# Optimization experiments

Hardware: AMD Instinct MI355X
Metric: run time of the kernel (lower is better)

The kernel has to match this reference:

```python
import jax, jax.numpy as jnp
import numpy as np

EPS = 1e-5

def instance_norm(x):
    # x: [B, n, C]; InstanceNorm1d normalizes over the n (length) axis per channel, no affine
    mean = jnp.mean(x, axis=1, keepdims=True)
    var = jnp.var(x, axis=1, keepdims=True)  # biased variance, matches torch
    return (x - mean) / jnp.sqrt(var + EPS)

def gat_layer(h, w, a_src, a_dst, b):
    # h: [B, n, d_in]; w: [H, d_in, d_out]; a_src/a_dst: [H, d_out, 1]; b: [d_out]
    h_ = jnp.einsum('bnd,hdk->bhnk', h, w)               # [B, H, n, d_out]
    s_src = jnp.einsum('bhnk,hk->bhn', h_, a_src[..., 0])  # [B, H, n]
    s_dst = jnp.einsum('bhnk,hk->bhn', h_, a_dst[..., 0])  # [B, H, n]
    attn = s_src[:, :, :, None] + s_dst[:, :, None, :]    # [B, H, n, n]
    attn = jax.nn.leaky_relu(attn, negative_slope=0.2)
    attn = jax.nn.softmax(attn, axis=-1)
    return jnp.einsum('bhnm,bhmk->bhnk', attn, h_) + b    # [B, H, n, d_out]

def setup_inputs() -> dict:
    key = jax.random.key(0)
    ks = jax.random.split(key, 7)
    B, N = 4, 4096
    x = jax.random.normal(ks[0], (B, N, 64), dtype=jnp.float32)
    g = 1.414
    def xavier(k, shape):
        fan_in, fan_out = shape[-2], shape[-1]
        lim = g * np.sqrt(6.0 / (fan_in + fan_out))
        return jax.random.uniform(k, shape, jnp.float32, -lim, lim)
    return {
        'x': x,
        'w0': xavier(ks[1], (4, 64, 32)),
        'a_src0': xavier(ks[2], (4, 32, 1)),
        'a_dst0': xavier(ks[3], (4, 32, 1)),
        'b0': jnp.zeros((32,), jnp.float32),
        'w1': xavier(ks[4], (1, 128, 64)),
        'a_src1': xavier(ks[5], (1, 64, 1)),
        'a_dst1': xavier(ks[6], (1, 64, 1)),
        'b1': jnp.zeros((64,), jnp.float32),
    }

def reference(x, w0, a_src0, a_dst0, b0, w1, a_src1, a_dst1, b1):
    B, N = x.shape[:2]
    # layer 0: norm -> GAT(4 heads) -> concat heads -> ELU
    h = instance_norm(x)
    h = gat_layer(h, w0, a_src0, a_dst0, b0)              # [B, 4, N, 32]
    h = jnp.transpose(h, (0, 2, 1, 3)).reshape(B, N, -1)  # [B, N, 128]
    h = jax.nn.elu(h)
    # layer 1: norm -> GAT(1 head) -> squeeze head
    h = instance_norm(h)
    h = gat_layer(h, w1, a_src1, a_dst1, b1)              # [B, 1, N, 64]
    return h[:, 0]                                        # [B, N, 64]
```

## Files before the change

### kernel.cpp

```cpp
#include <hip/hip_runtime.h>
#include <math.h>

#define N_ 4096

static constexpr size_t OFF_HP0    = 2048;
static constexpr size_t OFF_ELU    = 2048;
static constexpr size_t OFF_SS0    = 2099200;
static constexpr size_t OFF_SD0    = 2164736;
static constexpr size_t OFF_RUNS0  = 2230272;
static constexpr size_t OFF_SV0    = 2361344;
static constexpr size_t OFF_PM0    = 2426880;
static constexpr size_t OFF_EP0    = 2492416;
static constexpr size_t OFF_EN0    = 2557952;
static constexpr size_t OFF_CPP0   = 2623488;
static constexpr size_t OFF_CPN0   = 2689040;
static constexpr size_t OFF_TPP0   = 3279904;
static constexpr size_t OFF_TPN0   = 5377568;
static constexpr size_t OFF_HP1    = 3279904;
static constexpr size_t OFF_SS1    = 4328480;
static constexpr size_t OFF_SD1    = 4344864;
static constexpr size_t OFF_RUNS1  = 4361248;
static constexpr size_t OFF_SV1    = 4394016;
static constexpr size_t OFF_PM1    = 4410400;
static constexpr size_t OFF_EP1    = 4426784;
static constexpr size_t OFF_EN1    = 4443168;
static constexpr size_t OFF_CPP1   = 4459552;
static constexpr size_t OFF_CPN1   = 4475940;
static constexpr size_t OFF_TPP1   = 4754984;
static constexpr size_t OFF_TPN1   = 5803816;
static constexpr size_t OFF_S0P    = 7475232;
static constexpr size_t OFF_S1P    = 7491616;
static constexpr size_t OFF_RAWP0  = 7524384;
static constexpr size_t OFF_RAWN0  = 7786528;
static constexpr size_t OFF_BP0    = 8048672;
static constexpr size_t OFF_BN0    = 8311328;
static constexpr size_t OFF_RAWP1  = 8573984;
static constexpr size_t OFF_RAWN1  = 8705056;
static constexpr size_t OFF_BP1    = 8836128;
static constexpr size_t OFF_BN1    = 8967456;

__device__ __forceinline__ unsigned f2s(float f){
  unsigned u=__float_as_uint(f);
  return u^((u&0x80000000u)?0xFFFFFFFFu:0x80000000u);
}
__device__ __forceinline__ float s2f(unsigned s){
  unsigned u=(s&0x80000000u)?(s^0x80000000u):~s;
  return __uint_as_float(u);
}
__device__ __forceinline__ void fma4(float4& a, float s, float4 w){
  a.x+=s*w.x; a.y+=s*w.y; a.z+=s*w.z; a.w+=s*w.w;
}
__device__ __forceinline__ float dot4(float4 a, float4 b){
  return a.x*b.x+a.y*b.y+a.z*b.z+a.w*b.w;
}

template<int C>
__global__ void kstats(const float* __restrict__ x, float* __restrict__ statsP){
  int blk=blockIdx.x; int b=blk>>5;
  int tid=threadIdx.x;
  const int RPT=256/C;
  const int IT=128/RPT;
  int c=tid%C, rl=tid/C;
  const float* xb=x+(size_t)b*N_*C;
  float s1=0.f,s2=0.f;
  int r0=(blk&31)*128+rl;
  for(int i=0;i<IT;i++){
    float v=xb[(size_t)(r0+i*RPT)*C+c];
    s1+=v;s2+=v*v;
  }
  __shared__ float sh1[256],sh2[256];
  sh1[tid]=s1;sh2[tid]=s2;__syncthreads();
  if(tid<C){
    float a1=0.f,a2=0.f;
    for(int g=0;g<RPT;g++){a1+=sh1[g*C+tid];a2+=sh2[g*C+tid];}
    statsP[((size_t)blk*C+tid)*2+0]=a1;
    statsP[((size_t)blk*C+tid)*2+1]=a2;
  }
}

__global__ void __launch_bounds__(256) kproj0(
                       const float* __restrict__ x, const float* __restrict__ statsP,
                       const float* __restrict__ w0, const float* __restrict__ asrc,
                       const float* __restrict__ adst, float* __restrict__ hp,
                       float* __restrict__ ss, float* __restrict__ sd){
  __shared__ float4 w4[512];
  __shared__ float mean[64],rstd[64];
  __shared__ float red1[256],red2[256];
  __shared__ float ssP[1024],sdP[1024];
  int tid=threadIdx.x;
  int blk=blockIdx.x;
  int b=blk>>6, h=(blk>>4)&3, nb=blk&15;
  const float4* wg=(const float4*)w0+(size_t)h*512;
  w4[tid]=wg[tid]; w4[tid+256]=wg[tid+256];
  {
    int tc=tid&63, tg=tid>>6;
    float a1=0.f,a2=0.f;
    #pragma unroll 2
    for(int g=tg*8;g<tg*8+8;g++){
      a1+=statsP[((size_t)(b*32+g)*64+tc)*2+0];
      a2+=statsP[((size_t)(b*32+g)*64+tc)*2+1];
    }
    red1[tid]=a1; red2[tid]=a2;
  }
  __syncthreads();
  if(tid<64){
    float s1=red1[tid]+red1[tid+64]+red1[tid+128]+red1[tid+192];
    float s2=red2[tid]+red2[tid+64]+red2[tid+128]+red2[tid+192];
    float mu=s1*(1.0f/N_);
    float var=s2*(1.0f/N_)-mu*mu;
    mean[tid]=mu; rstd[tid]=rsqrtf(var+1e-5f);
  }
  __syncthreads();
  int w=tid>>6, lane=tid&63;
  int n0=nb*256+lane;
  const float4* xb=(const float4*)(x+((size_t)b*N_+n0)*64);
  float4 acc[4][2];
  #pragma unroll
  for(int r=0;r<4;r++){acc[r][0]=make_float4(0,0,0,0);acc[r][1]=make_float4(0,0,0,0);}
  for(int ch=0;ch<8;ch++){
    float4 wr[8][2];
    #pragma unroll
    for(int dd=0;dd<8;dd++){
      wr[dd][0]=w4[(ch*8+dd)*8+w*2+0];
      wr[dd][1]=w4[(ch*8+dd)*8+w*2+1];
    }
    float4 mn0=*(const float4*)&mean[ch*8], mn1=*(const float4*)&mean[ch*8+4];
    float4 rs0=*(const float4*)&rstd[ch*8], rs1=*(const float4*)&rstd[ch*8+4];
    #pragma unroll
    for(int r=0;r<4;r++){
      float4 t0=xb[(size_t)r*1024+ch*2+0];
      float4 t1=xb[(size_t)r*1024+ch*2+1];
      float hv[8];
      hv[0]=(t0.x-mn0.x)*rs0.x; hv[1]=(t0.y-mn0.y)*rs0.y;
      hv[2]=(t0.z-mn0.z)*rs0.z; hv[3]=(t0.w-mn0.w)*rs0.w;
      hv[4]=(t1.x-mn1.x)*rs1.x; hv[5]=(t1.y-mn1.y)*rs1.y;
      hv[6]=(t1.z-mn1.z)*rs1.z; hv[7]=(t1.w-mn1.w)*rs1.w;
      #pragma unroll
      for(int dd=0;dd<8;dd++){
        fma4(acc[r][0],hv[dd],wr[dd][0]);
        fma4(acc[r][1],hv[dd],wr[dd][1]);
      }
    }
  }
  float4 a1v0=((const float4*)asrc)[h*8+w*2+0];
  float4 a1v1=((const float4*)asrc)[h*8+w*2+1];
  float4 a2v0=((const float4*)adst)[h*8+w*2+0];
  float4 a2v1=((const float4*)adst)[h*8+w*2+1];
  int p=b*4+h;
  #pragma unroll
  for(int r=0;r<4;r++){
    ssP[w*256+r*64+lane]=dot4(acc[r][0],a1v0)+dot4(acc[r][1],a1v1);
    sdP[w*256+r*64+lane]=dot4(acc[r][0],a2v0)+dot4(acc[r][1],a2v1);
    float4* o4=(float4*)(hp+((size_t)p*N_+n0+r*64)*32+w*8);
    o4[0]=acc[r][0]; o4[1]=acc[r][1];
  }
  __syncthreads();
  {
    float s=ssP[tid]+ssP[256+tid]+ssP[512+tid]+ssP[768+tid];
    float d=sdP[tid]+sdP[256+tid]+sdP[512+tid]+sdP[768+tid];
    ss[(size_t)p*N_+nb*256+tid]=s;
    sd[(size_t)p*N_+nb*256+tid]=d;
  }
}

__global__ void __launch_bounds__(256) kproj1(
                       const float* __restrict__ x, const float* __restrict__ statsP,
                       const float* __restrict__ w1, const float* __restrict__ asrc,
                       const float* __restrict__ adst, float* __restrict__ hp,
                       float* __restrict__ ss, float* __restrict__ sd){
  __shared__ float4 w4[512];
  __shared__ float wa[128],wd[128],mean[128],rstd[128];
  __shared__ float red1[256],red2[256];
  int tid=threadIdx.x;
  int blk=blockIdx.x;
  int b=blk>>6, cgq=(blk>>4)&3, nb=blk&15;
  {
    const float4* wg=(const float4*)w1;
    int i=tid;       int d=i>>2, c=i&3; w4[i]=wg[d*16+cgq*4+c];
    i=tid+256;       d=i>>2;     c=i&3; w4[i]=wg[d*16+cgq*4+c];
  }
  {
    int tc=tid&127, tg=tid>>7;
    float a1=0.f,a2=0.f;
    #pragma unroll 4
    for(int g=tg*16;g<tg*16+16;g++){
      a1+=statsP[((size_t)(b*32+g)*128+tc)*2+0];
      a2+=statsP[((size_t)(b*32+g)*128+tc)*2+1];
    }
    red1[tid]=a1; red2[tid]=a2;
  }
  __syncthreads();
  if(tid<128){
    float s1a=0.f,s2a=0.f;
    for(int k=0;k<64;k++){float wv=w1[tid*64+k];s1a+=wv*asrc[k];s2a+=wv*adst[k];}
    wa[tid]=s1a;wd[tid]=s2a;
    float s1=red1[tid]+red1[tid+128];
    float s2=red2[tid]+red2[tid+128];
    float mu=s1*(1.0f/N_);
    float var=s2*(1.0f/N_)-mu*mu;
    mean[tid]=mu; rstd[tid]=rsqrtf(var+1e-5f);
  }
  __syncthreads();
  int w=tid>>6, lane=tid&63;
  int cg=cgq*4+w;
  int n0=nb*256+lane;
  const float4* xb=(const float4*)(x+((size_t)b*N_+n0)*128);
  float4 acc[4];
  #pragma unroll
  for(int r=0;r<4;r++) acc[r]=make_float4(0,0,0,0);
  float s1a[4]={0.f,0.f,0.f,0.f}, s2a[4]={0.f,0.f,0.f,0.f};
  bool dosum=(cgq==0)&&(w==0);
  for(int ch=0;ch<16;ch++){
    float4 wr[8];
    #pragma unroll
    for(int dd=0;dd<8;dd++) wr[dd]=w4[(ch*8+dd)*4+w];
    float4 mn0=*(const float4*)&mean[ch*8], mn1=*(const float4*)&mean[ch*8+4];
    float4 rs0=*(const float4*)&rstd[ch*8], rs1=*(const float4*)&rstd[ch*8+4];
    float4 wa0,wa1,wd0,wd1;
    if(dosum){
      wa0=*(const float4*)&wa[ch*8]; wa1=*(const float4*)&wa[ch*8+4];
      wd0=*(const float4*)&wd[ch*8]; wd1=*(const float4*)&wd[ch*8+4];
    }
    #pragma unroll
    for(int r=0;r<4;r++){
      float4 t0=xb[(size_t)r*2048+ch*2+0];
      float4 t1=xb[(size_t)r*2048+ch*2+1];
      float hv[8];
      hv[0]=(t0.x-mn0.x)*rs0.x; hv[1]=(t0.y-mn0.y)*rs0.y;
      hv[2]=(t0.z-mn0.z)*rs0.z; hv[3]=(t0.w-mn0.w)*rs0.w;
      hv[4]=(t1.x-mn1.x)*rs1.x; hv[5]=(t1.y-mn1.y)*rs1.y;
      hv[6]=(t1.z-mn1.z)*rs1.z; hv[7]=(t1.w-mn1.w)*rs1.w;
      #pragma unroll
      for(int dd=0;dd<8;dd++) fma4(acc[r],hv[dd],wr[dd]);
      if(dosum){
        s1a[r]+=hv[0]*wa0.x+hv[1]*wa0.y+hv[2]*wa0.z+hv[3]*wa0.w
               +hv[4]*wa1.x+hv[5]*wa1.y+hv[6]*wa1.z+hv[7]*wa1.w;
        s2a[r]+=hv[0]*wd0.x+hv[1]*wd0.y+hv[2]*wd0.z+hv[3]*wd0.w
               +hv[4]*wd1.x+hv[5]*wd1.y+hv[6]*wd1.z+hv[7]*wd1.w;
      }
    }
  }
  #pragma unroll
  for(int r=0;r<4;r++){
    float4* o4=(float4*)(hp+((size_t)b*N_+n0+r*64)*64+cg*4);
    o4[0]=acc[r];
  }
  if(dosum){
    #pragma unroll
    for(int r=0;r<4;r++){
      ss[(size_t)b*N_+n0+r*64]=s1a[r];
      sd[(size_t)b*N_+n0+r*64]=s2a[r];
    }
  }
}

__global__ void __launch_bounds__(512) ksort_runs(const float* __restrict__ sdst,
                                                  unsigned long long* __restrict__ runs){
  __shared__ unsigned long long sm[1024];
  int p=blockIdx.x>>2, run=blockIdx.x&3;
  int tid=threadIdx.x;
  const float* s=sdst+(size_t)p*N_+run*1024;
  for(int l=tid;l<1024;l+=512){
    unsigned key=f2s(s[l]);
    sm[l]=((unsigned long long)key<<32)|(unsigned)(run*1024+l);
  }
  for(unsigned k=2;k<=1024u;k<<=1)
    for(unsigned j=k>>1;j>0;j>>=1){
      __syncthreads();
      unsigned t=(unsigned)tid;
      unsigned i=((t&~(j-1))<<1)|(t&(j-1));
      unsigned q=i|j;
      bool up=((i&k)==0);
      unsigned long long a=sm[i],b=sm[q];
      if((a>b)==up){sm[i]=b;sm[q]=a;}
    }
  __syncthreads();
  unsigned long long* rg=runs+(size_t)p*N_+run*1024;
  for(int l=tid;l<1024;l+=512) rg[l]=sm[l];
}

__global__ void __launch_bounds__(1024) kmerge(const unsigned long long* __restrict__ runs,
    float* __restrict__ sv, unsigned* __restrict__ perm,
    float* __restrict__ eP, float* __restrict__ eN){
  __shared__ unsigned long long sm[4096];
  int p=blockIdx.x>>2, cg=blockIdx.x&3;
  int tid=threadIdx.x;
  const unsigned long long* rg=runs+(size_t)p*N_;
  for(int l=tid;l<4096;l+=1024) sm[l]=rg[l];
  __syncthreads();
  unsigned long long e=sm[cg*1024+tid];
  int rank=tid;
  #pragma unroll
  for(int o=0;o<4;o++){
    if(o==cg) continue;
    const unsigned long long* base=sm+o*1024;
    int lo=0,hi=1024;
    while(lo<hi){int mid=(lo+hi)>>1; if(base[mid]<e) lo=mid+1; else hi=mid;}
    rank+=lo;
  }
  unsigned long long mk=sm[1023];
  if(sm[2047]>mk) mk=sm[2047];
  if(sm[3071]>mk) mk=sm[3071];
  if(sm[4095]>mk) mk=sm[4095];
  float m=s2f((unsigned)(mk>>32));
  float v=s2f((unsigned)(e>>32));
  size_t o=(size_t)p*N_+rank;
  sv[o]=v;
  perm[o]=(unsigned)(e&0xffffffffu);
  eP[o]=expf(v-m);
  eN[o]=expf(0.2f*(v-m));
}

__device__ __forceinline__ void counts_block(const float* __restrict__ eP,
    const float* __restrict__ eN, float* __restrict__ CPP, float* __restrict__ CPN,
    int p, float* s){
  int t=threadIdx.x;
  for(int pass=0;pass<2;pass++){
    const float* e=pass?eN:eP;
    float* C=pass?CPN:CPP;
    const float4* e4=(const float4*)(e+(size_t)p*N_);
    float4 a0=e4[t*4+0],a1=e4[t*4+1],a2=e4[t*4+2],a3=e4[t*4+3];
    float lp=a0.x+a0.y+a0.z+a0.w+a1.x+a1.y+a1.z+a1.w
            +a2.x+a2.y+a2.z+a2.w+a3.x+a3.y+a3.z+a3.w;
    if(pass) __syncthreads();
    s[t]=lp; __syncthreads();
    for(int off=1;off<256;off<<=1){
      float tv=(t>=off)?s[t-off]:0.f;
      __syncthreads();
      s[t]+=tv;
      __syncthreads();
    }
    float bp=s[t]-lp;
    size_t o=(size_t)p*4097+(size_t)t*16;
    C[o+ 0]=bp; bp+=a0.x; C[o+ 1]=bp; bp+=a0.y; C[o+ 2]=bp; bp+=a0.z; C[o+ 3]=bp; bp+=a0.w;
    C[o+ 4]=bp; bp+=a1.x; C[o+ 5]=bp; bp+=a1.y; C[o+ 6]=bp; bp+=a1.z; C[o+ 7]=bp; bp+=a1.w;
    C[o+ 8]=bp; bp+=a2.x; C[o+ 9]=bp; bp+=a2.y; C[o+10]=bp; bp+=a2.z; C[o+11]=bp; bp+=a2.w;
    C[o+12]=bp; bp+=a3.x; C[o+13]=bp; bp+=a3.y; C[o+14]=bp; bp+=a3.z; C[o+15]=bp;
    if(t==255) C[(size_t)p*4097+4096]=s[255];
  }
}

__global__ void __launch_bounds__(256) ktables0(const unsigned* __restrict__ perm,
    const float* __restrict__ eP, const float* __restrict__ eN,
    const float* __restrict__ hp, float* __restrict__ TPP, float* __restrict__ TPN,
    float* __restrict__ rawP, float* __restrict__ rawN,
    float* __restrict__ CPP, float* __restrict__ CPN){
  __shared__ float s[256];
  if(blockIdx.x<16){ counts_block(eP,eN,CPP,CPN,blockIdx.x,s); return; }
  int gw=((blockIdx.x-16)*256+threadIdx.x)>>6;
  int lane=threadIdx.x&63, half=lane>>5, ch=lane&31;
  int cglob=gw*2+half;
  int p=cglob>>9, c=cglob&511;
  float aP=0.f,aN=0.f;
  #pragma unroll
  for(int q=0;q<8;q++){
    int r=c*8+q;
    size_t ro=(size_t)p*N_+r;
    float ep=eP[ro],en=eN[ro];
    unsigned pr=perm[ro];
    float hv=hp[((size_t)p*N_+pr)*32+ch];
    size_t to=((size_t)p*4097+r)*32+ch;
    TPP[to]=aP; TPN[to]=aN;
    aP+=ep*hv; aN+=en*hv;
  }
  size_t bo=((size_t)p*512+c)*32+ch;
  rawP[bo]=aP; rawN[bo]=aN;
}

__global__ void __launch_bounds__(256) ktables1(const unsigned* __restrict__ perm,
    const float* __restrict__ eP, const float* __restrict__ eN,
    const float* __restrict__ hp, float* __restrict__ TPP, float* __restrict__ TPN,
    float* __restrict__ rawP, float* __restrict__ rawN,
    float* __restrict__ CPP, float* __restrict__ CPN){
  __shared__ float s[256];
  if(blockIdx.x<4){ counts_block(eP,eN,CPP,CPN,blockIdx.x,s); return; }
  int wid=((blockIdx.x-4)*256+threadIdx.x)>>6;
  int lane=threadIdx.x&63;
  int p=wid>>9, c=wid&511;
  float aP=0.f,aN=0.f;
  #pragma unroll
  for(int q=0;q<8;q++){
    int r=c*8+q;
    size_t ro=(size_t)p*N_+r;
    float ep=eP[ro],en=eN[ro];
    unsigned pr=perm[ro];
    float hv=hp[((size_t)p*N_+pr)*64+lane];
    size_t to=((size_t)p*4097+r)*64+lane;
    TPP[to]=aP; TPN[to]=aN;
    aP+=ep*hv; aN+=en*hv;
  }
  size_t bo=((size_t)p*512+c)*64+lane;
  rawP[bo]=aP; rawN[bo]=aN;
}

template<int D>
__global__ void __launch_bounds__(256) kscan(const float* __restrict__ rawP,
    const float* __restrict__ rawN, float* __restrict__ bP, float* __restrict__ bN,
    float* __restrict__ TPP, float* __restrict__ TPN){
  __shared__ float ssum[256];
  int p=blockIdx.x>>1, pass=blockIdx.x&1;
  const float* src=pass?rawN:rawP;
  float* dst=pass?bN:bP;
  float* tp=pass?TPN:TPP;
  int tid=threadIdx.x;
  constexpr int SEG=256/D;
  constexpr int CPS=512/SEG;
  int ch=tid&(D-1), sg=tid/D;
  const float* s0=src+(size_t)p*512*D;
  float acc=0.f;
  for(int c=sg*CPS;c<sg*CPS+CPS;c++) acc+=s0[(size_t)c*D+ch];
  ssum[tid]=acc; __syncthreads();
  float base=0.f, tot=0.f;
  #pragma unroll
  for(int g=0;g<SEG;g++){float v=ssum[g*D+ch]; tot+=v; if(g<sg) base+=v;}
  float r=base;
  for(int c=sg*CPS;c<sg*CPS+CPS;c++){
    dst[((size_t)p*513+c)*D+ch]=r;
    r+=s0[(size_t)c*D+ch];
  }
  if(sg==0){
    dst[((size_t)p*513+512)*D+ch]=0.f;
    tp[((size_t)p*4097+4096)*D+ch]=tot;
  }
}

__global__ void __launch_bounds__(256) keval0(const float* __restrict__ ss,
                       const float* __restrict__ sv,
                       const float* __restrict__ bP, const float* __restrict__ bN,
                       const float* __restrict__ TPP, const float* __restrict__ TPN,
                       const float* __restrict__ CPP, const float* __restrict__ CPN,
                       const float* __restrict__ bias, float* __restrict__ out){
  __shared__ float svl[4128];
  __shared__ float ssl[32];
  int tid=threadIdx.x, blk=blockIdx.x;
  int p=blk>>7, i0=(blk&127)*32;
  int b=p>>2, h=p&3;
  const float* svp=sv+(size_t)p*N_;
  for(int j=tid;j<4096;j+=256) svl[j+(j>>7)]=svp[j];
  if(tid<32) ssl[tid]=ss[(size_t)p*N_+i0+tid];
  __syncthreads();
  int lane=tid&63, half=lane>>5, ch=lane&31;
  float bch=bias[ch];
  float m=svl[4126];
  float tot=TPP[((size_t)p*4097+4096)*32+ch];
  float CT =CPP[(size_t)p*4097+4096];
  for(int pass=0;pass<4;pass++){
    int rloc=pass*8+(tid>>5);
    int i=i0+rloc;
    float ssrc=ssl[rloc];
    float xx=ssrc+m;
    float M=xx>0.f?xx:0.2f*xx;
    float fpos=expf(xx-M),fneg=expf(0.2f*xx-M);
    float th=-ssrc;
    float s1v=svl[ch*129+127];
    unsigned long long bal=__ballot(s1v<=th);
    int c1=half?(int)__popcll(bal>>32):(int)__popcll(bal&0xFFFFFFFFull);
    int lo;
    if(c1>=32){ lo=4096; }
    else{
      float s2v=svl[c1*129+ch*4+3];
      unsigned long long bal2=__ballot(s2v<=th);
      int c2=half?(int)__popcll(bal2>>32):(int)__popcll(bal2&0xFFFFFFFFull);
      int base=c1*128+c2*4;
      int bi=base+c1;
      float q0=svl[bi],q1=svl[bi+1],q2=svl[bi+2],q3=svl[bi+3];
      int c3=(q0<=th)+(q1<=th)+(q2<=th)+(q3<=th);
      lo=base+c3;
    }
    int c=lo>>3;
    float relP=TPP[((size_t)p*4097+lo)*32+ch];
    float relN=TPN[((size_t)p*4097+lo)*32+ch];
    float baP=bP[((size_t)p*513+c)*32+ch];
    float baN=bN[((size_t)p*513+c)*32+ch];
    float CPl=CPP[(size_t)p*4097+lo];
    float CNl=CPN[(size_t)p*4097+lo];
    float denom=fpos*(CT-CPl)+fneg*CNl;
    float v=fpos*(tot-(baP+relP))+fneg*(baN+relN);
    float r=v/denom+bch;
    r=r>0.f?r:expm1f(r);
    out[((size_t)(b*N_+i))*128+h*32+ch]=r;
  }
}

__global__ void __launch_bounds__(256) keval1(const float* __restrict__ ss,
                       const float* __restrict__ sv,
                       const float* __restrict__ bP, const float* __restrict__ bN,
                       const float* __restrict__ TPP, const float* __restrict__ TPN,
                       const float* __restrict__ CPP, const float* __restrict__ CPN,
                       const float* __restrict__ bias, float* __restrict__ out){
  __shared__ float svl[4160];
  __shared__ float ssl[32];
  int tid=threadIdx.x, blk=blockIdx.x;
  int p=blk>>7, i0=(blk&127)*32;
  const float* svp=sv+(size_t)p*N_;
  for(int j=tid;j<4096;j+=256) svl[j+(j>>6)]=svp[j];
  if(tid<32) ssl[tid]=ss[(size_t)p*N_+i0+tid];
  __syncthreads();
  int lane=tid&63;
  float bch=bias[lane];
  float m=svl[4158];
  float tot=TPP[((size_t)p*4097+4096)*64+lane];
  float CT =CPP[(size_t)p*4097+4096];
  for(int pass=0;pass<8;pass++){
    int rloc=pass*4+(tid>>6);
    int i=i0+rloc;
    float ssrc=ssl[rloc];
    float xx=ssrc+m;
    float M=xx>0.f?xx:0.2f*xx;
    float fpos=expf(xx-M),fneg=expf(0.2f*xx-M);
    float th=-ssrc;
    float s1v=svl[lane*65+63];
    int c1=(int)__popcll(__ballot(s1v<=th));
    int lo;
    if(c1>=64){ lo=4096; }
    else{
      float s2v=svl[c1*65+lane];
      lo=c1*64+(int)__popcll(__ballot(s2v<=th));
    }
    int c=lo>>3;
    float relP=TPP[((size_t)p*4097+lo)*64+lane];
    float relN=TPN[((size_t)p*4097+lo)*64+lane];
    float baP=bP[((size_t)p*513+c)*64+lane];
    float baN=bN[((size_t)p*513+c)*64+lane];
    float CPl=CPP[(size_t)p*4097+lo];
    float CNl=CPN[(size_t)p*4097+lo];
    float denom=fpos*(CT-CPl)+fneg*CNl;
    float v=fpos*(tot-(baP+relP))+fneg*(baN+relN);
    out[((size_t)p*N_+i)*64+lane]=v/denom+bch;
  }
}

extern "C" void kernel_launch(void* const* d_in, const int* in_sizes, int n_in,
                              void* d_out, int out_size, void* d_ws, size_t ws_size,
                              hipStream_t stream) {
  const float* x  =(const float*)d_in[0];
  const float* w0 =(const float*)d_in[1];
  const float* as0=(const float*)d_in[2];
  const float* ad0=(const float*)d_in[3];
  const float* b0 =(const float*)d_in[4];
  const float* w1 =(const float*)d_in[5];
  const float* as1=(const float*)d_in[6];
  const float* ad1=(const float*)d_in[7];
  const float* b1 =(const float*)d_in[8];
  float* ws=(float*)d_ws;
  float* out=(float*)d_out;

  float* s0p = ws+OFF_S0P;
  float* s1p = ws+OFF_S1P;
  float* hp0 = ws+OFF_HP0;
  float* elu = ws+OFF_ELU;
  float* ss0 = ws+OFF_SS0;  float* sd0 = ws+OFF_SD0;
  unsigned long long* runs0=(unsigned long long*)(ws+OFF_RUNS0);
  float* sv0 = ws+OFF_SV0;
  unsigned* pm0=(unsigned*)(ws+OFF_PM0);
  float* eP0 = ws+OFF_EP0;  float* eN0 = ws+OFF_EN0;
  float* cP0 = ws+OFF_CPP0; float* cN0 = ws+OFF_CPN0;
  float* rP0 = ws+OFF_RAWP0; float* rN0 = ws+OFF_RAWN0;
  float* bP0 = ws+OFF_BP0;  float* bN0 = ws+OFF_BN0;
  float* tP0 = ws+OFF_TPP0; float* tN0 = ws+OFF_TPN0;
  float* hp1 = ws+OFF_HP1;
  float* ss1 = ws+OFF_SS1;  float* sd1 = ws+OFF_SD1;
  unsigned long long* runs1=(unsigned long long*)(ws+OFF_RUNS1);
  float* sv1 = ws+OFF_SV1;
  unsigned* pm1=(unsigned*)(ws+OFF_PM1);
  float* eP1 = ws+OFF_EP1;  float* eN1 = ws+OFF_EN1;
  float* cP1 = ws+OFF_CPP1; float* cN1 = ws+OFF_CPN1;
  float* rP1 = ws+OFF_RAWP1; float* rN1 = ws+OFF_RAWN1;
  float* bP1 = ws+OFF_BP1;  float* bN1 = ws+OFF_BN1;
  float* tP1 = ws+OFF_TPP1; float* tN1 = ws+OFF_TPN1;

  kstats<64><<<128,256,0,stream>>>(x,s0p);
  kproj0<<<256,256,0,stream>>>(x,s0p,w0,as0,ad0,hp0,ss0,sd0);
  ksort_runs<<<64,512,0,stream>>>(sd0,runs0);
  kmerge<<<64,1024,0,stream>>>(runs0,sv0,pm0,eP0,eN0);
  ktables0<<<1040,256,0,stream>>>(pm0,eP0,eN0,hp0,tP0,tN0,rP0,rN0,cP0,cN0);
  kscan<32><<<32,256,0,stream>>>(rP0,rN0,bP0,bN0,tP0,tN0);
  keval0<<<2048,256,0,stream>>>(ss0,sv0,bP0,bN0,tP0,tN0,cP0,cN0,b0,elu);
  kstats<128><<<128,256,0,stream>>>(elu,s1p);
  kproj1<<<256,256,0,stream>>>(elu,s1p,w1,as1,ad1,hp1,ss1,sd1);
  ksort_runs<<<16,512,0,stream>>>(sd1,runs1);
  kmerge<<<16,1024,0,stream>>>(runs1,sv1,pm1,eP1,eN1);
  ktables1<<<516,256,0,stream>>>(pm1,eP1,eN1,hp1,tP1,tN1,rP1,rN1,cP1,cN1);
  kscan<64><<<8,256,0,stream>>>(rP1,rN1,bP1,bN1,tP1,tN1);
  keval1<<<512,256,0,stream>>>(ss1,sv1,bP1,bN1,tP1,tN1,cP1,cN1,b1,out);
}
```

Before: 192.7 us.

## Interleave P/N prefix tables as float2 and fuse layer-1 stats into keval0

After: 207.0 us. +7.4%, slower.

```diff
diff --git a/kernel.cpp b/kernel.cpp
--- a/kernel.cpp
+++ b/kernel.cpp
@@ -12,10 +12,8 @@
 static constexpr size_t OFF_PM0    = 2426880;
 static constexpr size_t OFF_EP0    = 2492416;
 static constexpr size_t OFF_EN0    = 2557952;
-static constexpr size_t OFF_CPP0   = 2623488;
-static constexpr size_t OFF_CPN0   = 2689040;
-static constexpr size_t OFF_TPP0   = 3279904;
-static constexpr size_t OFF_TPN0   = 5377568;
+static constexpr size_t OFF_CP0    = 2623488;
+static constexpr size_t OFF_TP0    = 3279904;
 static constexpr size_t OFF_HP1    = 3279904;
 static constexpr size_t OFF_SS1    = 4328480;
 static constexpr size_t OFF_SD1    = 4344864;
@@ -24,20 +22,14 @@
 static constexpr size_t OFF_PM1    = 4410400;
 static constexpr size_t OFF_EP1    = 4426784;
 static constexpr size_t OFF_EN1    = 4443168;
-static constexpr size_t OFF_CPP1   = 4459552;
-static constexpr size_t OFF_CPN1   = 4475940;
-static constexpr size_t OFF_TPP1   = 4754984;
-static constexpr size_t OFF_TPN1   = 5803816;
+static constexpr size_t OFF_CP1    = 4459552;
+static constexpr size_t OFF_TP1    = 4754984;
 static constexpr size_t OFF_S0P    = 7475232;
-static constexpr size_t OFF_S1P    = 7491616;
-static constexpr size_t OFF_RAWP0  = 7524384;
-static constexpr size_t OFF_RAWN0  = 7786528;
-static constexpr size_t OFF_BP0    = 8048672;
-static constexpr size_t OFF_BN0    = 8311328;
-static constexpr size_t OFF_RAWP1  = 8573984;
-static constexpr size_t OFF_RAWN1  = 8705056;
-static constexpr size_t OFF_BP1    = 8836128;
-static constexpr size_t OFF_BN1    = 8967456;
+static constexpr size_t OFF_RAW0   = 7524384;
+static constexpr size_t OFF_B0     = 8048672;
+static constexpr size_t OFF_RAW1   = 8573984;
+static constexpr size_t OFF_B1     = 8836128;
+static constexpr size_t OFF_EVP    = 9098784;
 
 __device__ __forceinline__ unsigned f2s(float f){
   unsigned u=__float_as_uint(f);
@@ -164,7 +156,7 @@
 }
 
 __global__ void __launch_bounds__(256) kproj1(
-                       const float* __restrict__ x, const float* __restrict__ statsP,
+                       const float* __restrict__ x, const float* __restrict__ evp,
                        const float* __restrict__ w1, const float* __restrict__ asrc,
                        const float* __restrict__ adst, float* __restrict__ hp,
                        float* __restrict__ ss, float* __restrict__ sd){
@@ -181,11 +173,14 @@
   }
   {
     int tc=tid&127, tg=tid>>7;
+    int hh=tc>>5, ch=tc&31;
+    int p=b*4+hh;
     float a1=0.f,a2=0.f;
     #pragma unroll 4
-    for(int g=tg*16;g<tg*16+16;g++){
-      a1+=statsP[((size_t)(b*32+g)*128+tc)*2+0];
-      a2+=statsP[((size_t)(b*32+g)*128+tc)*2+1];
+    for(int rg=tg*64;rg<tg*64+64;rg++){
+      size_t eo=(((size_t)p*128+rg)*32+ch)*2;
+      a1+=evp[eo+0];
+      a2+=evp[eo+1];
     }
     red1[tid]=a1; red2[tid]=a2;
   }
@@ -312,12 +307,10 @@
 }
 
 __device__ __forceinline__ void counts_block(const float* __restrict__ eP,
-    const float* __restrict__ eN, float* __restrict__ CPP, float* __restrict__ CPN,
-    int p, float* s){
+    const float* __restrict__ eN, float* __restrict__ CP, int p, float* s){
   int t=threadIdx.x;
   for(int pass=0;pass<2;pass++){
     const float* e=pass?eN:eP;
-    float* C=pass?CPN:CPP;
     const float4* e4=(const float4*)(e+(size_t)p*N_);
     float4 a0=e4[t*4+0],a1=e4[t*4+1],a2=e4[t*4+2],a3=e4[t*4+3];
     float lp=a0.x+a0.y+a0.z+a0.w+a1.x+a1.y+a1.z+a1.w
@@ -331,22 +324,21 @@
       __syncthreads();
     }
     float bp=s[t]-lp;
-    size_t o=(size_t)p*4097+(size_t)t*16;
-    C[o+ 0]=bp; bp+=a0.x; C[o+ 1]=bp; bp+=a0.y; C[o+ 2]=bp; bp+=a0.z; C[o+ 3]=bp; bp+=a0.w;
-    C[o+ 4]=bp; bp+=a1.x; C[o+ 5]=bp; bp+=a1.y; C[o+ 6]=bp; bp+=a1.z; C[o+ 7]=bp; bp+=a1.w;
-    C[o+ 8]=bp; bp+=a2.x; C[o+ 9]=bp; bp+=a2.y; C[o+10]=bp; bp+=a2.z; C[o+11]=bp; bp+=a2.w;
-    C[o+12]=bp; bp+=a3.x; C[o+13]=bp; bp+=a3.y; C[o+14]=bp; bp+=a3.z; C[o+15]=bp;
-    if(t==255) C[(size_t)p*4097+4096]=s[255];
+    size_t o=((size_t)p*4097+(size_t)t*16)*2+pass;
+    CP[o+ 0]=bp; bp+=a0.x; CP[o+ 2]=bp; bp+=a0.y; CP[o+ 4]=bp; bp+=a0.z; CP[o+ 6]=bp; bp+=a0.w;
+    CP[o+ 8]=bp; bp+=a1.x; CP[o+10]=bp; bp+=a1.y; CP[o+12]=bp; bp+=a1.z; CP[o+14]=bp; bp+=a1.w;
+    CP[o+16]=bp; bp+=a2.x; CP[o+18]=bp; bp+=a2.y; CP[o+20]=bp; bp+=a2.z; CP[o+22]=bp; bp+=a2.w;
+    CP[o+24]=bp; bp+=a3.x; CP[o+26]=bp; bp+=a3.y; CP[o+28]=bp; bp+=a3.z; CP[o+30]=bp;
+    if(t==255) CP[((size_t)p*4097+4096)*2+pass]=s[255];
   }
 }
 
 __global__ void __launch_bounds__(256) ktables0(const unsigned* __restrict__ perm,
     const float* __restrict__ eP, const float* __restrict__ eN,
-    const float* __restrict__ hp, float* __restrict__ TPP, float* __restrict__ TPN,
-    float* __restrict__ rawP, float* __restrict__ rawN,
-    float* __restrict__ CPP, float* __restrict__ CPN){
+    const float* __restrict__ hp, float2* __restrict__ TP2,
+    float2* __restrict__ raw2, float* __restrict__ CP){
   __shared__ float s[256];
-  if(blockIdx.x<16){ counts_block(eP,eN,CPP,CPN,blockIdx.x,s); return; }
+  if(blockIdx.x<16){ counts_block(eP,eN,CP,blockIdx.x,s); return; }
   int gw=((blockIdx.x-16)*256+threadIdx.x)>>6;
   int lane=threadIdx.x&63, half=lane>>5, ch=lane&31;
   int cglob=gw*2+half;
@@ -359,21 +351,18 @@
     float ep=eP[ro],en=eN[ro];
     unsigned pr=perm[ro];
     float hv=hp[((size_t)p*N_+pr)*32+ch];
-    size_t to=((size_t)p*4097+r)*32+ch;
-    TPP[to]=aP; TPN[to]=aN;
+    TP2[((size_t)p*4097+r)*32+ch]=make_float2(aP,aN);
     aP+=ep*hv; aN+=en*hv;
   }
-  size_t bo=((size_t)p*512+c)*32+ch;
-  rawP[bo]=aP; rawN[bo]=aN;
+  raw2[((size_t)p*512+c)*32+ch]=make_float2(aP,aN);
 }
 
 __global__ void __launch_bounds__(256) ktables1(const unsigned* __restrict__ perm,
     const float* __restrict__ eP, const float* __restrict__ eN,
-    const float* __restrict__ hp, float* __restrict__ TPP, float* __restrict__ TPN,
-    float* __restrict__ rawP, float* __restrict__ rawN,
-    float* __restrict__ CPP, float* __restrict__ CPN){
+    const float* __restrict__ hp, float2* __restrict__ TP2,
+    float2* __restrict__ raw2, float* __restrict__ CP){
   __shared__ float s[256];
-  if(blockIdx.x<4){ counts_block(eP,eN,CPP,CPN,blockIdx.x,s); return; }
+  if(blockIdx.x<4){ counts_block(eP,eN,CP,blockIdx.x,s); return; }
   int wid=((blockIdx.x-4)*256+threadIdx.x)>>6;
   int lane=threadIdx.x&63;
   int p=wid>>9, c=wid&511;
@@ -385,65 +374,65 @@
     float ep=eP[ro],en=eN[ro];
     unsigned pr=perm[ro];
     float hv=hp[((size_t)p*N_+pr)*64+lane];
-    size_t to=((size_t)p*4097+r)*64+lane;
-    TPP[to]=aP; TPN[to]=aN;
+    TP2[((size_t)p*4097+r)*64+lane]=make_float2(aP,aN);
     aP+=ep*hv; aN+=en*hv;
   }
-  size_t bo=((size_t)p*512+c)*64+lane;
-  rawP[bo]=aP; rawN[bo]=aN;
+  raw2[((size_t)p*512+c)*64+lane]=make_float2(aP,aN);
 }
 
 template<int D>
-__global__ void __launch_bounds__(256) kscan(const float* __restrict__ rawP,
-    const float* __restrict__ rawN, float* __restrict__ bP, float* __restrict__ bN,
-    float* __restrict__ TPP, float* __restrict__ TPN){
-  __shared__ float ssum[256];
-  int p=blockIdx.x>>1, pass=blockIdx.x&1;
-  const float* src=pass?rawN:rawP;
-  float* dst=pass?bN:bP;
-  float* tp=pass?TPN:TPP;
-  int tid=threadIdx.x;
+__global__ void __launch_bounds__(256) kscan(const float2* __restrict__ raw,
+    float2* __restrict__ B, float2* __restrict__ TP){
+  __shared__ float sx[256],sy[256];
+  int p=blockIdx.x, tid=threadIdx.x;
   constexpr int SEG=256/D;
   constexpr int CPS=512/SEG;
   int ch=tid&(D-1), sg=tid/D;
-  const float* s0=src+(size_t)p*512*D;
-  float acc=0.f;
-  for(int c=sg*CPS;c<sg*CPS+CPS;c++) acc+=s0[(size_t)c*D+ch];
-  ssum[tid]=acc; __syncthreads();
-  float base=0.f, tot=0.f;
-  #pragma unroll
-  for(int g=0;g<SEG;g++){float v=ssum[g*D+ch]; tot+=v; if(g<sg) base+=v;}
-  float r=base;
+  const float2* s0=raw+(size_t)p*512*D;
+  float ax=0.f,ay=0.f;
+  for(int c=sg*CPS;c<sg*CPS+CPS;c++){float2 v=s0[(size_t)c*D+ch];ax+=v.x;ay+=v.y;}
+  sx[tid]=ax; sy[tid]=ay; __syncthreads();
+  float bx=0.f,by=0.f,tx=0.f,ty=0.f;
+  #pragma unroll
+  for(int g=0;g<SEG;g++){
+    float vx=sx[g*D+ch],vy=sy[g*D+ch];
+    tx+=vx;ty+=vy;
+    if(g<sg){bx+=vx;by+=vy;}
+  }
+  float rx=bx,ry=by;
   for(int c=sg*CPS;c<sg*CPS+CPS;c++){
-    dst[((size_t)p*513+c)*D+ch]=r;
-    r+=s0[(size_t)c*D+ch];
+    B[((size_t)p*513+c)*D+ch]=make_float2(rx,ry);
+    float2 v=s0[(size_t)c*D+ch]; rx+=v.x; ry+=v.y;
   }
   if(sg==0){
-    dst[((size_t)p*513+512)*D+ch]=0.f;
-    tp[((size_t)p*4097+4096)*D+ch]=tot;
+    B[((size_t)p*513+512)*D+ch]=make_float2(0.f,0.f);
+    TP[((size_t)p*4097+4096)*D+ch]=make_float2(tx,ty);
   }
 }
 
 __global__ void __launch_bounds__(256) keval0(const float* __restrict__ ss,
                        const float* __restrict__ sv,
-                       const float* __restrict__ bP, const float* __restrict__ bN,
-                       const float* __restrict__ TPP, const float* __restrict__ TPN,
-                       const float* __restrict__ CPP, const float* __restrict__ CPN,
-                       const float* __restrict__ bias, float* __restrict__ out){
+                       const float2* __restrict__ B2, const float2* __restrict__ TP2,
+                       const float2* __restrict__ CP2,
+                       const float* __restrict__ bias, float* __restrict__ out,
+                       float* __restrict__ evp){
   __shared__ float svl[4128];
   __shared__ float ssl[32];
+  __shared__ float sm1[256],sm2[256];
   int tid=threadIdx.x, blk=blockIdx.x;
-  int p=blk>>7, i0=(blk&127)*32;
+  int p=blk>>7, rg=blk&127;
+  int i0=rg*32;
   int b=p>>2, h=p&3;
   const float* svp=sv+(size_t)p*N_;
   for(int j=tid;j<4096;j+=256) svl[j+(j>>7)]=svp[j];
   if(tid<32) ssl[tid]=ss[(size_t)p*N_+i0+tid];
   __syncthreads();
-  int lane=tid&63, half=lane>>5, ch=lane&31;
+  int lane=tid&63, half=lane>>5, ch=tid&31;
   float bch=bias[ch];
   float m=svl[4126];
-  float tot=TPP[((size_t)p*4097+4096)*32+ch];
-  float CT =CPP[(size_t)p*4097+4096];
+  float tot=TP2[((size_t)p*4097+4096)*32+ch].x;
+  float CT =CP2[(size_t)p*4097+4096].x;
+  float s1=0.f,s2=0.f;
   for(int pass=0;pass<4;pass++){
     int rloc=pass*8+(tid>>5);
     int i=i0+rloc;
@@ -468,25 +457,31 @@
       lo=base+c3;
     }
     int c=lo>>3;
-    float relP=TPP[((size_t)p*4097+lo)*32+ch];
-    float relN=TPN[((size_t)p*4097+lo)*32+ch];
-    float baP=bP[((size_t)p*513+c)*32+ch];
-    float baN=bN[((size_t)p*513+c)*32+ch];
-    float CPl=CPP[(size_t)p*4097+lo];
-    float CNl=CPN[(size_t)p*4097+lo];
-    float denom=fpos*(CT-CPl)+fneg*CNl;
-    float v=fpos*(tot-(baP+relP))+fneg*(baN+relN);
+    float2 rel=TP2[((size_t)p*4097+lo)*32+ch];
+    float2 ba =B2[((size_t)p*513+c)*32+ch];
+    float2 cp =CP2[(size_t)p*4097+lo];
+    float denom=fpos*(CT-cp.x)+fneg*cp.y;
+    float v=fpos*(tot-(ba.x+rel.x))+fneg*(ba.y+rel.y);
     float r=v/denom+bch;
     r=r>0.f?r:expm1f(r);
     out[((size_t)(b*N_+i))*128+h*32+ch]=r;
+    s1+=r; s2+=r*r;
+  }
+  sm1[tid]=s1; sm2[tid]=s2;
+  __syncthreads();
+  if(tid<32){
+    float a1=0.f,a2=0.f;
+    #pragma unroll
+    for(int g=0;g<8;g++){a1+=sm1[g*32+tid];a2+=sm2[g*32+tid];}
+    size_t eo=(((size_t)p*128+rg)*32+tid)*2;
+    evp[eo+0]=a1; evp[eo+1]=a2;
   }
 }
 
 __global__ void __launch_bounds__(256) keval1(const float* __restrict__ ss,
                        const float* __restrict__ sv,
-                       const float* __restrict__ bP, const float* __restrict__ bN,
-                       const float* __restrict__ TPP, const float* __restrict__ TPN,
-                       const float* __restrict__ CPP, const float* __restrict__ CPN,
+                       const float2* __restrict__ B2, const float2* __restrict__ TP2,
+                       const float2* __restrict__ CP2,
                        const float* __restrict__ bias, float* __restrict__ out){
   __shared__ float svl[4160];
   __shared__ float ssl[32];
@@ -499,8 +494,8 @@
   int lane=tid&63;
   float bch=bias[lane];
   float m=svl[4158];
-  float tot=TPP[((size_t)p*4097+4096)*64+lane];
-  float CT =CPP[(size_t)p*4097+4096];
+  float tot=TP2[((size_t)p*4097+4096)*64+lane].x;
+  float CT =CP2[(size_t)p*4097+4096].x;
   for(int pass=0;pass<8;pass++){
     int rloc=pass*4+(tid>>6);
     int i=i0+rloc;
@@ -518,14 +513,11 @@
       lo=c1*64+(int)__popcll(__ballot(s2v<=th));
     }
     int c=lo>>3;
-    float relP=TPP[((size_t)p*4097+lo)*64+lane];
-    float relN=TPN[((size_t)p*4097+lo)*64+lane];
-    float baP=bP[((size_t)p*513+c)*64+lane];
-    float baN=bN[((size_t)p*513+c)*64+lane];
-    float CPl=CPP[(size_t)p*4097+lo];
-    float CNl=CPN[(size_t)p*4097+lo];
-    float denom=fpos*(CT-CPl)+fneg*CNl;
-    float v=fpos*(tot-(baP+relP))+fneg*(baN+relN);
+    float2 rel=TP2[((size_t)p*4097+lo)*64+lane];
+    float2 ba =B2[((size_t)p*513+c)*64+lane];
+    float2 cp =CP2[(size_t)p*4097+lo];
+    float denom=fpos*(CT-cp.x)+fneg*cp.y;
+    float v=fpos*(tot-(ba.x+rel.x))+fneg*(ba.y+rel.y);
     out[((size_t)p*N_+i)*64+lane]=v/denom+bch;
   }
 }
@@ -546,7 +538,7 @@
   float* out=(float*)d_out;
 
   float* s0p = ws+OFF_S0P;
-  float* s1p = ws+OFF_S1P;
+  float* evp = ws+OFF_EVP;
   float* hp0 = ws+OFF_HP0;
   float* elu = ws+OFF_ELU;
   float* ss0 = ws+OFF_SS0;  float* sd0 = ws+OFF_SD0;
@@ -554,33 +546,32 @@
   float* sv0 = ws+OFF_SV0;
   unsigned* pm0=(unsigned*)(ws+OFF_PM0);
   float* eP0 = ws+OFF_EP0;  float* eN0 = ws+OFF_EN0;
-  float* cP0 = ws+OFF_CPP0; float* cN0 = ws+OFF_CPN0;
-  float* rP0 = ws+OFF_RAWP0; float* rN0 = ws+OFF_RAWN0;
-  float* bP0 = ws+OFF_BP0;  float* bN0 = ws+OFF_BN0;
-  float* tP0 = ws+OFF_TPP0; float* tN0 = ws+OFF_TPN0;
+  float* cp0 = ws+OFF_CP0;
+  float2* raw0=(float2*)(ws+OFF_RAW0);
+  float2* bb0 =(float2*)(ws+OFF_B0);
+  float2* tp0 =(float2*)(ws+OFF_TP0);
   float* hp1 = ws+OFF_HP1;
   float* ss1 = ws+OFF_SS1;  float* sd1 = ws+OFF_SD1;
   unsigned long long* runs1=(unsigned long long*)(ws+OFF_RUNS1);
   float* sv1 = ws+OFF_SV1;
   unsigned* pm1=(unsigned*)(ws+OFF_PM1);
   float* eP1 = ws+OFF_EP1;  float* eN1 = ws+OFF_EN1;
-  float* cP1 = ws+OFF_CPP1; float* cN1 = ws+OFF_CPN1;
-  float* rP1 = ws+OFF_RAWP1; float* rN1 = ws+OFF_RAWN1;
-  float* bP1 = ws+OFF_BP1;  float* bN1 = ws+OFF_BN1;
-  float* tP1 = ws+OFF_TPP1; float* tN1 = ws+OFF_TPN1;
+  float* cp1 = ws+OFF_CP1;
+  float2* raw1=(float2*)(ws+OFF_RAW1);
+  float2* bb1 =(float2*)(ws+OFF_B1);
+  float2* tp1 =(float2*)(ws+OFF_TP1);
 
   kstats<64><<<128,256,0,stream>>>(x,s0p);
   kproj0<<<256,256,0,stream>>>(x,s0p,w0,as0,ad0,hp0,ss0,sd0);
   ksort_runs<<<64,512,0,stream>>>(sd0,runs0);
   kmerge<<<64,1024,0,stream>>>(runs0,sv0,pm0,eP0,eN0);
-  ktables0<<<1040,256,0,stream>>>(pm0,eP0,eN0,hp0,tP0,tN0,rP0,rN0,cP0,cN0);
-  kscan<32><<<32,256,0,stream>>>(rP0,rN0,bP0,bN0,tP0,tN0);
-  keval0<<<2048,256,0,stream>>>(ss0,sv0,bP0,bN0,tP0,tN0,cP0,cN0,b0,elu);
-  kstats<128><<<128,256,0,stream>>>(elu,s1p);
-  kproj1<<<256,256,0,stream>>>(elu,s1p,w1,as1,ad1,hp1,ss1,sd1);
+  ktables0<<<1040,256,0,stream>>>(pm0,eP0,eN0,hp0,tp0,raw0,cp0);
+  kscan<32><<<16,256,0,stream>>>(raw0,bb0,tp0);
+  keval0<<<2048,256,0,stream>>>(ss0,sv0,bb0,tp0,(const float2*)cp0,b0,elu,evp);
+  kproj1<<<256,256,0,stream>>>(elu,evp,w1,as1,ad1,hp1,ss1,sd1);
   ksort_runs<<<16,512,0,stream>>>(sd1,runs1);
   kmerge<<<16,1024,0,stream>>>(runs1,sv1,pm1,eP1,eN1);
-  ktables1<<<516,256,0,stream>>>(pm1,eP1,eN1,hp1,tP1,tN1,rP1,rN1,cP1,cN1);
-  kscan<64><<<8,256,0,stream>>>(rP1,rN1,bP1,bN1,tP1,tN1);
-  keval1<<<512,256,0,stream>>>(ss1,sv1,bP1,bN1,tP1,tN1,cP1,cN1,b1,out);
-}
+  ktables1<<<516,256,0,stream>>>(pm1,eP1,eN1,hp1,tp1,raw1,cp1);
+  kscan<64><<<4,256,0,stream>>>(raw1,bb1,tp1);
+  keval1<<<512,256,0,stream>>>(ss1,sv1,bb1,tp1,(const float2*)cp1,b1,out);
+}
```
